# Kernel tuning notes

Hardware: AMD Instinct MI355X
Metric: run time of the kernel (lower is better)

## Reference

```python
import jax, jax.numpy as jnp
import numpy as np

B, T, I, H = 256, 4096, 1, 32

def setup_inputs() -> dict:
    key = jax.random.key(0)
    ks = jax.random.split(key, 7)
    s = 1.0 / np.sqrt(H)
    return {
        "x": jax.random.normal(ks[0], (B, T, I), dtype=jnp.float32),
        "W_ih": jax.random.uniform(ks[1], (H, I), minval=-s, maxval=s, dtype=jnp.float32),
        "W_hh": jax.random.uniform(ks[2], (H, H), minval=-s, maxval=s, dtype=jnp.float32),
        "b_ih": jax.random.uniform(ks[3], (H,), minval=-s, maxval=s, dtype=jnp.float32),
        "b_hh": jax.random.uniform(ks[4], (H,), minval=-s, maxval=s, dtype=jnp.float32),
        "W_fc": jax.random.uniform(ks[5], (1, H), minval=-s, maxval=s, dtype=jnp.float32),
        "b_fc": jax.random.uniform(ks[6], (1,), minval=-s, maxval=s, dtype=jnp.float32),
    }

def reference(x, W_ih, W_hh, b_ih, b_hh, W_fc, b_fc):
    # Precompute input projection for all timesteps: [B,T,H]
    xp = jnp.einsum('bti,hi->bth', x, W_ih) + b_ih + b_hh
    h0 = jnp.zeros((x.shape[0], W_hh.shape[0]), dtype=x.dtype)

    def step(h, xp_t):
        h = jnp.tanh(xp_t + h @ W_hh.T)  # [B,H]
        return h, h

    _, hs = jax.lax.scan(step, h0, jnp.swapaxes(xp, 0, 1))  # hs: [T,B,H]
    out = jnp.swapaxes(hs, 0, 1)  # [B,T,H]
    return jnp.einsum('bth,oh->bto', out, W_fc) + b_fc  # [B,T,1]
```

## Files before the change

### kernel.cpp

```cpp
#include <hip/hip_runtime.h>
#include <math.h>

#define NB 256
#define TT 4096
#define HH 32
#define CH 64

#if __has_builtin(__builtin_amdgcn_exp2f)
#define EXP2F(x) __builtin_amdgcn_exp2f(x)
#else
#define EXP2F(x) exp2f(x)
#endif

__device__ __forceinline__ float rlane(float v, int l) {
    return __uint_as_float(__builtin_amdgcn_readlane(__float_as_uint(v), l));
}

__global__ __launch_bounds__(64, 1) void rnn_fused(
    const float* __restrict__ x,
    const float* __restrict__ W_ih,
    const float* __restrict__ W_hh,
    const float* __restrict__ b_ih,
    const float* __restrict__ b_hh,
    const float* __restrict__ W_fc,
    const float* __restrict__ b_fc,
    float* __restrict__ out)
{
    const int lane = threadIdx.x;
    const int i16  = lane & 15;
    const int R    = lane >> 4;
    const int j    = lane & 31;
    const int kh   = (R ^ (R >> 1)) & 1;

    __shared__ float obuf[64 * 65];

    const float KAPPA = 2.8853900817779268f;

    int rr;
    asm volatile("s_nop 1\n\t"
                 "v_mov_b32_dpp %0, %1 row_ror:1 row_mask:0xf bank_mask:0xf"
                 : "=v"(rr) : "v"(lane));
    const int rsign = ((rr & 15) == ((i16 + 1) & 15)) ? 1 : -1;

    int va = lane, vb = lane;
    asm volatile("s_nop 1\n\t"
                 "v_permlane16_swap_b32 %0, %1" : "+v"(va), "+v"(vb));
    const int  tgt  = kh * 16 + i16;
    const bool useA = ((va & 31) == tgt);

    float rowsum = 0.0f;
#pragma unroll
    for (int k = 0; k < HH; ++k) rowsum += W_hh[j * HH + k];

    float Wd[16];
#pragma unroll
    for (int d = 0; d < 16; ++d)
        Wd[d] = -2.0f * KAPPA * W_hh[j * HH + kh * 16 + ((i16 + rsign * d) & 15)];

    const float wihH  = 0.5f * KAPPA * W_ih[j];
    const float biasH = 0.5f * KAPPA * (b_ih[j] + b_hh[j] + rowsum);

    float wfcm[HH];
    float sum_wfc = 0.0f;
#pragma unroll
    for (int r = 0; r < HH; ++r) {
        float w = W_fc[r];
        sum_wfc += w;
        wfcm[r] = -2.0f * w;
    }
    const float bfc2 = b_fc[0] + sum_wfc;

    const size_t xbase = (size_t)blockIdx.x * TT;
    float xv = x[xbase + lane];
    float rv = 0.5f;

    for (int c = 0; c < TT / CH; ++c) {
        const int cn = (c + 1) & (TT / CH - 1);
        float xv_next = x[xbase + cn * CH + lane];

#pragma unroll 8
        for (int tc = 0; tc < CH; ++tc) {
            float sx   = rlane(xv, tc);
            float acc0 = fmaf(wihH, sx, biasH);
            float acc1 = 0.0f, acc2 = 0.0f, acc3 = 0.0f;

            asm("s_nop 1\n\t"
                "v_fmac_f32 %0, %4, %5\n\t"
                "v_fmac_f32_dpp %1, %4, %6 row_ror:1 row_mask:0xf bank_mask:0xf\n\t"
                "v_fmac_f32_dpp %2, %4, %7 row_ror:2 row_mask:0xf bank_mask:0xf\n\t"
                "v_fmac_f32_dpp %3, %4, %8 row_ror:3 row_mask:0xf bank_mask:0xf\n\t"
                "v_fmac_f32_dpp %0, %4, %9 row_ror:4 row_mask:0xf bank_mask:0xf\n\t"
                "v_fmac_f32_dpp %1, %4, %10 row_ror:5 row_mask:0xf bank_mask:0xf\n\t"
                "v_fmac_f32_dpp %2, %4, %11 row_ror:6 row_mask:0xf bank_mask:0xf\n\t"
                "v_fmac_f32_dpp %3, %4, %12 row_ror:7 row_mask:0xf bank_mask:0xf\n\t"
                "v_fmac_f32_dpp %0, %4, %13 row_ror:8 row_mask:0xf bank_mask:0xf\n\t"
                "v_fmac_f32_dpp %1, %4, %14 row_ror:9 row_mask:0xf bank_mask:0xf\n\t"
                "v_fmac_f32_dpp %2, %4, %15 row_ror:10 row_mask:0xf bank_mask:0xf\n\t"
                "v_fmac_f32_dpp %3, %4, %16 row_ror:11 row_mask:0xf bank_mask:0xf\n\t"
                "v_fmac_f32_dpp %0, %4, %17 row_ror:12 row_mask:0xf bank_mask:0xf\n\t"
                "v_fmac_f32_dpp %1, %4, %18 row_ror:13 row_mask:0xf bank_mask:0xf\n\t"
                "v_fmac_f32_dpp %2, %4, %19 row_ror:14 row_mask:0xf bank_mask:0xf\n\t"
                "v_fmac_f32_dpp %3, %4, %20 row_ror:15 row_mask:0xf bank_mask:0xf"
                : "+v"(acc0), "+v"(acc1), "+v"(acc2), "+v"(acc3)
                : "v"(rv),
                  "v"(Wd[0]),  "v"(Wd[1]),  "v"(Wd[2]),  "v"(Wd[3]),
                  "v"(Wd[4]),  "v"(Wd[5]),  "v"(Wd[6]),  "v"(Wd[7]),
                  "v"(Wd[8]),  "v"(Wd[9]),  "v"(Wd[10]), "v"(Wd[11]),
                  "v"(Wd[12]), "v"(Wd[13]), "v"(Wd[14]), "v"(Wd[15]));

            float p = (acc0 + acc1) + (acc2 + acc3);

            float u = p, w2 = p;
            asm("s_nop 1\n\t"
                "v_permlane32_swap_b32 %0, %1" : "+v"(u), "+v"(w2));
            float dot = u + w2;

            float e   = EXP2F(dot);
            float rnw = __builtin_amdgcn_rcpf(e + 1.0f);

            float fa = rnw, fb = rnw;
            asm("s_nop 2\n\t"
                "v_permlane16_swap_b32 %0, %1" : "+v"(fa), "+v"(fb));
            rv = useA ? fa : fb;

            obuf[lane * 65 + tc] = rnw;
        }

        __builtin_amdgcn_wave_barrier();
        float s0 = 0.0f, s1 = 0.0f, s2 = 0.0f, s3 = 0.0f;
#pragma unroll
        for (int r = 0; r < HH; r += 4) {
            s0 = fmaf(obuf[(r + 0) * 65 + lane], wfcm[r + 0], s0);
            s1 = fmaf(obuf[(r + 1) * 65 + lane], wfcm[r + 1], s1);
            s2 = fmaf(obuf[(r + 2) * 65 + lane], wfcm[r + 2], s2);
            s3 = fmaf(obuf[(r + 3) * 65 + lane], wfcm[r + 3], s3);
        }
        out[xbase + c * CH + lane] = (s0 + s1) + (s2 + s3) + bfc2;

        xv = xv_next;
        __builtin_amdgcn_wave_barrier();
    }
}

extern "C" void kernel_launch(void* const* d_in, const int* in_sizes, int n_in,
                              void* d_out, int out_size, void* d_ws, size_t ws_size,
                              hipStream_t stream) {
    const float* x    = (const float*)d_in[0];
    const float* W_ih = (const float*)d_in[1];
    const float* W_hh = (const float*)d_in[2];
    const float* b_ih = (const float*)d_in[3];
    const float* b_hh = (const float*)d_in[4];
    const float* W_fc = (const float*)d_in[5];
    const float* b_fc = (const float*)d_in[6];
    float* out = (float*)d_out;

    rnn_fused<<<NB, 64, 0, stream>>>(x, W_ih, W_hh, b_ih, b_hh, W_fc, b_fc, out);
}
```

Before: 386.8 us.

## Pack two batch rows per wave, one hidden unit per lane

Each 64-lane wave now processes two batch sequences, with each half-wave owning all 32 hidden units of one sequence. The per-step matvec becomes two 16-wide DPP FMA chains (own row half and swapped other half) instead of splitting the dot product across halves and reducing with permlane32. This halves the grid to 128 blocks and shrinks the chunk size to 32 timesteps. The per-step serial chain gets 16 more dependent FMAs but drops the permlane32 reduction, and the total number of waves is halved.

```diff
diff --git a/kernel.cpp b/kernel.cpp
--- a/kernel.cpp
+++ b/kernel.cpp
@@ -1,10 +1,10 @@
 #include <hip/hip_runtime.h>
 #include <math.h>
 
-#define NB 256
+#define NBLK 128
 #define TT 4096
 #define HH 32
-#define CH 64
+#define CH 32
 
 #if __has_builtin(__builtin_amdgcn_exp2f)
 #define EXP2F(x) __builtin_amdgcn_exp2f(x)
@@ -28,9 +28,10 @@
 {
     const int lane = threadIdx.x;
     const int i16  = lane & 15;
-    const int R    = lane >> 4;
-    const int j    = lane & 31;
-    const int kh   = (R ^ (R >> 1)) & 1;
+    const int hl   = lane & 31;
+    const int half = lane >> 5;
+    const int row  = (hl >> 4) & 1;
+    const int j    = hl;
 
     __shared__ float obuf[64 * 65];
 
@@ -45,20 +46,24 @@
     int va = lane, vb = lane;
     asm volatile("s_nop 1\n\t"
                  "v_permlane16_swap_b32 %0, %1" : "+v"(va), "+v"(vb));
-    const int  tgt  = kh * 16 + i16;
-    const bool useA = ((va & 31) == tgt);
+    const bool useA = (((va ^ lane) >> 4) & 1) != 0;
 
     float rowsum = 0.0f;
 #pragma unroll
     for (int k = 0; k < HH; ++k) rowsum += W_hh[j * HH + k];
 
-    float Wd[16];
+    const int ownb = row * 16;
+    const int othb = 16 - ownb;
+
+    float Wo[16], Wq[16];
 #pragma unroll
-    for (int d = 0; d < 16; ++d)
-        Wd[d] = -2.0f * KAPPA * W_hh[j * HH + kh * 16 + ((i16 + rsign * d) & 15)];
+    for (int d = 0; d < 16; ++d) {
+        Wo[d] = -2.0f * KAPPA * W_hh[j * HH + ownb + ((i16 + rsign * d) & 15)];
+        Wq[d] = -2.0f * KAPPA * W_hh[j * HH + othb + ((i16 + rsign * d) & 15)];
+    }
 
-    const float wihH  = 0.5f * KAPPA * W_ih[j];
-    const float biasH = 0.5f * KAPPA * (b_ih[j] + b_hh[j] + rowsum);
+    const float wih  = KAPPA * W_ih[j];
+    const float bias = KAPPA * (b_ih[j] + b_hh[j] + rowsum);
 
     float wfcm[HH];
     float sum_wfc = 0.0f;
@@ -70,19 +75,27 @@
     }
     const float bfc2 = b_fc[0] + sum_wfc;
 
-    const size_t xbase = (size_t)blockIdx.x * TT;
-    float xv = x[xbase + lane];
+    const size_t xb = ((size_t)blockIdx.x * 2 + half) * TT;
+    float xv = x[xb + hl];
     float rv = 0.5f;
 
     for (int c = 0; c < TT / CH; ++c) {
         const int cn = (c + 1) & (TT / CH - 1);
-        float xv_next = x[xbase + cn * CH + lane];
+        float xv_next = x[xb + cn * CH + hl];
 
 #pragma unroll 8
         for (int tc = 0; tc < CH; ++tc) {
-            float sx   = rlane(xv, tc);
-            float acc0 = fmaf(wihH, sx, biasH);
+            float sxA = rlane(xv, tc);
+            float sxB = rlane(xv, 32 + tc);
+            float sx  = half ? sxB : sxA;
+
+            float acc0 = fmaf(wih, sx, bias);
             float acc1 = 0.0f, acc2 = 0.0f, acc3 = 0.0f;
+
+            float fa = rv, fb = rv;
+            asm("s_nop 1\n\t"
+                "v_permlane16_swap_b32 %0, %1" : "+v"(fa), "+v"(fb));
+            float rvO = useA ? fa : fb;
 
             asm("s_nop 1\n\t"
                 "v_fmac_f32 %0, %4, %5\n\t"
@@ -103,26 +116,40 @@
                 "v_fmac_f32_dpp %3, %4, %20 row_ror:15 row_mask:0xf bank_mask:0xf"
                 : "+v"(acc0), "+v"(acc1), "+v"(acc2), "+v"(acc3)
                 : "v"(rv),
-                  "v"(Wd[0]),  "v"(Wd[1]),  "v"(Wd[2]),  "v"(Wd[3]),
-                  "v"(Wd[4]),  "v"(Wd[5]),  "v"(Wd[6]),  "v"(Wd[7]),
-                  "v"(Wd[8]),  "v"(Wd[9]),  "v"(Wd[10]), "v"(Wd[11]),
-                  "v"(Wd[12]), "v"(Wd[13]), "v"(Wd[14]), "v"(Wd[15]));
+                  "v"(Wo[0]),  "v"(Wo[1]),  "v"(Wo[2]),  "v"(Wo[3]),
+                  "v"(Wo[4]),  "v"(Wo[5]),  "v"(Wo[6]),  "v"(Wo[7]),
+                  "v"(Wo[8]),  "v"(Wo[9]),  "v"(Wo[10]), "v"(Wo[11]),
+                  "v"(Wo[12]), "v"(Wo[13]), "v"(Wo[14]), "v"(Wo[15]));
+
+            asm("v_fmac_f32 %0, %4, %5\n\t"
+                "v_fmac_f32_dpp %1, %4, %6 row_ror:1 row_mask:0xf bank_mask:0xf\n\t"
+                "v_fmac_f32_dpp %2, %4, %7 row_ror:2 row_mask:0xf bank_mask:0xf\n\t"
+                "v_fmac_f32_dpp %3, %4, %8 row_ror:3 row_mask:0xf bank_mask:0xf\n\t"
+                "v_fmac_f32_dpp %0, %4, %9 row_ror:4 row_mask:0xf bank_mask:0xf\n\t"
+                "v_fmac_f32_dpp %1, %4, %10 row_ror:5 row_mask:0xf bank_mask:0xf\n\t"
+                "v_fmac_f32_dpp %2, %4, %11 row_ror:6 row_mask:0xf bank_mask:0xf\n\t"
+                "v_fmac_f32_dpp %3, %4, %12 row_ror:7 row_mask:0xf bank_mask:0xf\n\t"
+                "v_fmac_f32_dpp %0, %4, %13 row_ror:8 row_mask:0xf bank_mask:0xf\n\t"
+                "v_fmac_f32_dpp %1, %4, %14 row_ror:9 row_mask:0xf bank_mask:0xf\n\t"
+                "v_fmac_f32_dpp %2, %4, %15 row_ror:10 row_mask:0xf bank_mask:0xf\n\t"
+                "v_fmac_f32_dpp %3, %4, %16 row_ror:11 row_mask:0xf bank_mask:0xf\n\t"
+                "v_fmac_f32_dpp %0, %4, %17 row_ror:12 row_mask:0xf bank_mask:0xf\n\t"
+                "v_fmac_f32_dpp %1, %4, %18 row_ror:13 row_mask:0xf bank_mask:0xf\n\t"
+                "v_fmac_f32_dpp %2, %4, %19 row_ror:14 row_mask:0xf bank_mask:0xf\n\t"
+                "v_fmac_f32_dpp %3, %4, %20 row_ror:15 row_mask:0xf bank_mask:0xf"
+                : "+v"(acc0), "+v"(acc1), "+v"(acc2), "+v"(acc3)
+                : "v"(rvO),
+                  "v"(Wq[0]),  "v"(Wq[1]),  "v"(Wq[2]),  "v"(Wq[3]),
+                  "v"(Wq[4]),  "v"(Wq[5]),  "v"(Wq[6]),  "v"(Wq[7]),
+                  "v"(Wq[8]),  "v"(Wq[9]),  "v"(Wq[10]), "v"(Wq[11]),
+                  "v"(Wq[12]), "v"(Wq[13]), "v"(Wq[14]), "v"(Wq[15]));
 
             float p = (acc0 + acc1) + (acc2 + acc3);
 
-            float u = p, w2 = p;
-            asm("s_nop 1\n\t"
-                "v_permlane32_swap_b32 %0, %1" : "+v"(u), "+v"(w2));
-            float dot = u + w2;
-
-            float e   = EXP2F(dot);
+            float e   = EXP2F(p);
             float rnw = __builtin_amdgcn_rcpf(e + 1.0f);
 
-            float fa = rnw, fb = rnw;
-            asm("s_nop 2\n\t"
-                "v_permlane16_swap_b32 %0, %1" : "+v"(fa), "+v"(fb));
-            rv = useA ? fa : fb;
-
+            rv = rnw;
             obuf[lane * 65 + tc] = rnw;
         }
 
@@ -130,12 +157,12 @@
         float s0 = 0.0f, s1 = 0.0f, s2 = 0.0f, s3 = 0.0f;
 #pragma unroll
         for (int r = 0; r < HH; r += 4) {
-            s0 = fmaf(obuf[(r + 0) * 65 + lane], wfcm[r + 0], s0);
-            s1 = fmaf(obuf[(r + 1) * 65 + lane], wfcm[r + 1], s1);
-            s2 = fmaf(obuf[(r + 2) * 65 + lane], wfcm[r + 2], s2);
-            s3 = fmaf(obuf[(r + 3) * 65 + lane], wfcm[r + 3], s3);
+            s0 = fmaf(obuf[(32 * half + r + 0) * 65 + hl], wfcm[r + 0], s0);
+            s1 = fmaf(obuf[(32 * half + r + 1) * 65 + hl], wfcm[r + 1], s1);
+            s2 = fmaf(obuf[(32 * half + r + 2) * 65 + hl], wfcm[r + 2], s2);
+            s3 = fmaf(obuf[(32 * half + r + 3) * 65 + hl], wfcm[r + 3], s3);
         }
-        out[xbase + c * CH + lane] = (s0 + s1) + (s2 + s3) + bfc2;
+        out[xb + c * CH + hl] = (s0 + s1) + (s2 + s3) + bfc2;
 
         xv = xv_next;
         __builtin_amdgcn_wave_barrier();
@@ -154,5 +181,5 @@
     const float* b_fc = (const float*)d_in[6];
     float* out = (float*)d_out;
 
-    rnn_fused<<<NB, 64, 0, stream>>>(x, W_ih, W_hh, b_ih, b_hh, W_fc, b_fc, out);
+    rnn_fused<<<NBLK, 64, 0, stream>>>(x, W_ih, W_hh, b_ih, b_hh, W_fc, b_fc, out);
 }
```

After: 503.0 us. +30.0%, slower.
